# Kernel tuning notes

Measured on AMD Instinct MI355X. Metric: run time of the kernel, lower is better.

Reference implementation:

```python
import jax, jax.numpy as jnp
import numpy as np

DIM = 512

def setup_inputs() -> dict:
    key = jax.random.key(0)
    k1, k2 = jax.random.split(key)
    pq = jax.random.normal(k1, (65536, 2 * DIM), dtype=jnp.float32)
    A = jax.random.normal(k2, (DIM, DIM), dtype=jnp.float32)
    return {"pq": pq, "A": A}

def reference(pq, A):
    # up_or_low == 'up': p' = p + (A + A^T) q ; q' = q
    S = A + A.T  # symmetric (dim, dim)
    p = pq[..., :DIM]
    q = pq[..., DIM:]
    # (A+A^T) q for each row: since S is symmetric, q @ S == q @ S^T
    pterm = jnp.einsum('bd,ed->be', q, S)  # matches mv(S, q) per row
    return jnp.concatenate([p + pterm, q], axis=-1)
```

## Files before the change

### kernel.cpp

```cpp
#include <hip/hip_runtime.h>
#include <hip/hip_bf16.h>

#define DIM 512
#define BM 64
#define BK 32
#define LSTRIDE 40

typedef __bf16 bf16x8 __attribute__((ext_vector_type(8)));
typedef float f32x16 __attribute__((ext_vector_type(16)));

union B128 { uint4 u; bf16x8 v; };

__device__ __forceinline__ unsigned short f2bf(float f) {
    union { __hip_bfloat16 b; unsigned short u; } c;
    c.b = __float2bfloat16(f);
    return c.u;
}

__global__ void prep_s_kernel(const float* __restrict__ A,
                              unsigned short* __restrict__ S) {
    int i = blockIdx.x * 256 + threadIdx.x;
    int e = i >> 9;
    int d = i & 511;
    S[i] = f2bf(A[e * DIM + d] + A[d * DIM + e]);
}

__global__ __launch_bounds__(512, 4) void fused_gemm_kernel(
        const float* __restrict__ pq,
        const unsigned short* __restrict__ S,
        float* __restrict__ out) {
    __shared__ __align__(16) unsigned short qs[BM * LSTRIDE];
    __shared__ __align__(16) unsigned short ss[DIM * LSTRIDE];

    const int t = threadIdx.x;
    const int l = t & 63;
    const int w = t >> 6;
    const int wm = w >> 2;
    const int wn = w & 3;
    const int half = l >> 5;
    const int lane31 = l & 31;
    const int m0 = blockIdx.x * BM;

    f32x16 acc[4];
    #pragma unroll
    for (int nt = 0; nt < 4; ++nt)
        #pragma unroll
        for (int r = 0; r < 16; ++r) acc[nt][r] = 0.0f;

    const int qrow = t >> 3;
    const int qcol = (t & 7) * 4;

    for (int kc = 0; kc < DIM / BK; ++kc) {
        const int k0 = kc * BK;

        const size_t qoff = (size_t)(m0 + qrow) * (2 * DIM) + DIM + k0 + qcol;
        float4 qv = *(const float4*)(pq + qoff);
        *(float4*)(out + qoff) = qv;

        if (kc) __syncthreads();

        ushort4 qb;
        qb.x = f2bf(qv.x); qb.y = f2bf(qv.y); qb.z = f2bf(qv.z); qb.w = f2bf(qv.w);
        *(ushort4*)&qs[qrow * LSTRIDE + qcol] = qb;

        #pragma unroll
        for (int i = 0; i < 4; ++i) {
            int ch = i * 512 + t;
            int srow = ch >> 2;
            int scol = (ch & 3) * 8;
            uint4 sv = *(const uint4*)(S + (size_t)srow * DIM + k0 + scol);
            *(uint4*)&ss[srow * LSTRIDE + scol] = sv;
        }
        __syncthreads();

        B128 a0, a1;
        const int arow = 32 * wm + lane31;
        a0.u = *(const uint4*)&qs[arow * LSTRIDE + half * 8];
        a1.u = *(const uint4*)&qs[arow * LSTRIDE + 16 + half * 8];
        #pragma unroll
        for (int nt = 0; nt < 4; ++nt) {
            const int brow = 128 * nt + 32 * wn + lane31;
            B128 b0, b1;
            b0.u = *(const uint4*)&ss[brow * LSTRIDE + half * 8];
            b1.u = *(const uint4*)&ss[brow * LSTRIDE + 16 + half * 8];
            acc[nt] = __builtin_amdgcn_mfma_f32_32x32x16_bf16(a0.v, b0.v, acc[nt], 0, 0, 0);
            acc[nt] = __builtin_amdgcn_mfma_f32_32x32x16_bf16(a1.v, b1.v, acc[nt], 0, 0, 0);
        }
    }

    #pragma unroll
    for (int nt = 0; nt < 4; ++nt) {
        const int col = 128 * nt + 32 * wn + lane31;
        #pragma unroll
        for (int r = 0; r < 16; ++r) {
            const int row = m0 + 32 * wm + 4 * half + (r & 3) + 8 * (r >> 2);
            const size_t off = (size_t)row * (2 * DIM) + col;
            out[off] = pq[off] + acc[nt][r];
        }
    }
}

extern "C" void kernel_launch(void* const* d_in, const int* in_sizes, int n_in,
                              void* d_out, int out_size, void* d_ws, size_t ws_size,
                              hipStream_t stream) {
    const float* pq = (const float*)d_in[0];
    const float* A  = (const float*)d_in[1];
    float* out = (float*)d_out;
    unsigned short* S = (unsigned short*)d_ws;

    prep_s_kernel<<<(DIM * DIM) / 256, 256, 0, stream>>>(A, S);
    fused_gemm_kernel<<<65536 / BM, 512, 0, stream>>>(pq, S, out);
}
```

Measured before the change: 515.7 us.

## Drop LDS staging and load MFMA operands directly from global memory

The GEMM kernel no longer stages q and S tiles in shared memory with barriers. Each lane now loads its MFMA A and B fragments straight from global memory, relying on L1/L2 caching of the small bf16 S matrix. Blocks shrink to 4 waves, each computing 32x256 with 8 accumulators. This removes the LDS traffic and __syncthreads, but it raises global and L2 load traffic, makes loads uncoalesced (16 bytes per row per lane), and doubles accumulator registers.

```diff
diff --git a/kernel.cpp b/kernel.cpp
--- a/kernel.cpp
+++ b/kernel.cpp
@@ -2,14 +2,11 @@
 #include <hip/hip_bf16.h>
 
 #define DIM 512
-#define BM 64
-#define BK 32
-#define LSTRIDE 40
 
 typedef __bf16 bf16x8 __attribute__((ext_vector_type(8)));
 typedef float f32x16 __attribute__((ext_vector_type(16)));
 
-union B128 { uint4 u; bf16x8 v; };
+union B128 { uint4 u; bf16x8 v; unsigned short us[8]; };
 
 __device__ __forceinline__ unsigned short f2bf(float f) {
     union { __hip_bfloat16 b; unsigned short u; } c;
@@ -25,72 +22,56 @@
     S[i] = f2bf(A[e * DIM + d] + A[d * DIM + e]);
 }
 
-__global__ __launch_bounds__(512, 4) void fused_gemm_kernel(
+__global__ __launch_bounds__(256, 2) void fused_gemm_kernel(
         const float* __restrict__ pq,
         const unsigned short* __restrict__ S,
         float* __restrict__ out) {
-    __shared__ __align__(16) unsigned short qs[BM * LSTRIDE];
-    __shared__ __align__(16) unsigned short ss[DIM * LSTRIDE];
-
     const int t = threadIdx.x;
     const int l = t & 63;
     const int w = t >> 6;
-    const int wm = w >> 2;
-    const int wn = w & 3;
+    const int wm = w >> 1;
+    const int nh = w & 1;
     const int half = l >> 5;
     const int lane31 = l & 31;
-    const int m0 = blockIdx.x * BM;
+    const int m0 = blockIdx.x * 64;
 
-    f32x16 acc[4];
+    const int arow = m0 + 32 * wm + lane31;
+    const float* qptr = pq + (size_t)arow * (2 * DIM) + DIM;
+    float* qout = out + (size_t)arow * (2 * DIM) + DIM;
+
+    f32x16 acc[8];
     #pragma unroll
-    for (int nt = 0; nt < 4; ++nt)
+    for (int nt = 0; nt < 8; ++nt)
         #pragma unroll
         for (int r = 0; r < 16; ++r) acc[nt][r] = 0.0f;
 
-    const int qrow = t >> 3;
-    const int qcol = (t & 7) * 4;
-
-    for (int kc = 0; kc < DIM / BK; ++kc) {
-        const int k0 = kc * BK;
-
-        const size_t qoff = (size_t)(m0 + qrow) * (2 * DIM) + DIM + k0 + qcol;
-        float4 qv = *(const float4*)(pq + qoff);
-        *(float4*)(out + qoff) = qv;
-
-        if (kc) __syncthreads();
-
-        ushort4 qb;
-        qb.x = f2bf(qv.x); qb.y = f2bf(qv.y); qb.z = f2bf(qv.z); qb.w = f2bf(qv.w);
-        *(ushort4*)&qs[qrow * LSTRIDE + qcol] = qb;
+    #pragma unroll 4
+    for (int kc = 0; kc < DIM / 16; ++kc) {
+        const int k = kc * 16 + half * 8;
+        float4 av0 = *(const float4*)(qptr + k);
+        float4 av1 = *(const float4*)(qptr + k + 4);
+        if (nh == 0) {
+            *(float4*)(qout + k) = av0;
+            *(float4*)(qout + k + 4) = av1;
+        }
+        B128 af;
+        af.us[0] = f2bf(av0.x); af.us[1] = f2bf(av0.y);
+        af.us[2] = f2bf(av0.z); af.us[3] = f2bf(av0.w);
+        af.us[4] = f2bf(av1.x); af.us[5] = f2bf(av1.y);
+        af.us[6] = f2bf(av1.z); af.us[7] = f2bf(av1.w);
 
         #pragma unroll
-        for (int i = 0; i < 4; ++i) {
-            int ch = i * 512 + t;
-            int srow = ch >> 2;
-            int scol = (ch & 3) * 8;
-            uint4 sv = *(const uint4*)(S + (size_t)srow * DIM + k0 + scol);
-            *(uint4*)&ss[srow * LSTRIDE + scol] = sv;
-        }
-        __syncthreads();
-
-        B128 a0, a1;
-        const int arow = 32 * wm + lane31;
-        a0.u = *(const uint4*)&qs[arow * LSTRIDE + half * 8];
-        a1.u = *(const uint4*)&qs[arow * LSTRIDE + 16 + half * 8];
-        #pragma unroll
-        for (int nt = 0; nt < 4; ++nt) {
-            const int brow = 128 * nt + 32 * wn + lane31;
-            B128 b0, b1;
-            b0.u = *(const uint4*)&ss[brow * LSTRIDE + half * 8];
-            b1.u = *(const uint4*)&ss[brow * LSTRIDE + 16 + half * 8];
-            acc[nt] = __builtin_amdgcn_mfma_f32_32x32x16_bf16(a0.v, b0.v, acc[nt], 0, 0, 0);
-            acc[nt] = __builtin_amdgcn_mfma_f32_32x32x16_bf16(a1.v, b1.v, acc[nt], 0, 0, 0);
+        for (int nt = 0; nt < 8; ++nt) {
+            const int n = nh * 256 + nt * 32 + lane31;
+            B128 bf;
+            bf.u = *(const uint4*)(S + (size_t)n * DIM + k);
+            acc[nt] = __builtin_amdgcn_mfma_f32_32x32x16_bf16(af.v, bf.v, acc[nt], 0, 0, 0);
         }
     }
 
     #pragma unroll
-    for (int nt = 0; nt < 4; ++nt) {
-        const int col = 128 * nt + 32 * wn + lane31;
+    for (int nt = 0; nt < 8; ++nt) {
+        const int col = nh * 256 + nt * 32 + lane31;
         #pragma unroll
         for (int r = 0; r < 16; ++r) {
             const int row = m0 + 32 * wm + 4 * half + (r & 3) + 8 * (r >> 2);
@@ -109,5 +90,5 @@
     unsigned short* S = (unsigned short*)d_ws;
 
     prep_s_kernel<<<(DIM * DIM) / 256, 256, 0, stream>>>(A, S);
-    fused_gemm_kernel<<<65536 / BM, 512, 0, stream>>>(pq, S, out);
+    fused_gemm_kernel<<<65536 / 64, 256, 0, stream>>>(pq, S, out);
 }
```

New measurement: 726.2 us. 1.41x slower.
